# Kernel optimization log

Hardware: AMD Instinct MI355X
Metric: run time of the kernel (lower is better)

Reference implementation:

```python
import jax, jax.numpy as jnp
import numpy as np

N = 100000      # nodes == in_ch (transductive: x = arange(N))
E = 3200000     # nonzeros of sparse hypergraph adjacency G (COO)
D = 128         # i_emb
DROPOUT = 0.1


def setup_inputs() -> dict:
    key = jax.random.key(0)
    k1, k2, k3, k4, k5 = jax.random.split(key, 5)
    x = jnp.arange(N, dtype=jnp.int64) if jax.config.jax_enable_x64 else jnp.arange(N, dtype=jnp.int32)
    row = jax.random.randint(k1, (E,), 0, N, dtype=jnp.int32)
    col = jax.random.randint(k2, (E,), 0, N, dtype=jnp.int32)
    vals = jax.random.uniform(k3, (E,), dtype=jnp.float32)
    # xavier-uniform embedding: bound = sqrt(6/(N+D))
    eb = float(np.sqrt(6.0 / (N + D)))
    embed_w = jax.random.uniform(k4, (N, D), jnp.float32, -eb, eb)
    fb = float(np.sqrt(6.0 / (D + D)))
    fc_w = jax.random.uniform(k5, (D, D), jnp.float32, -fb, fb)
    fc_b = jnp.zeros((D,), jnp.float32)
    return {"x": x, "row": row, "col": col, "vals": vals,
            "embed_w": embed_w, "fc_w": fc_w, "fc_b": fc_b}


def reference(x, row, col, vals, embed_w, fc_w, fc_b):
    e = embed_w[x]                                   # [N, D] embedding lookup
    # SpMM: out[i] = sum_{nz} vals * e[col]  scattered to row
    agg = jax.ops.segment_sum(vals[:, None] * e[col], row, num_segments=e.shape[0])
    m1 = agg + e                                     # residual
    keep = 1.0 - DROPOUT                             # F.dropout (training=True default)
    mask = jax.random.bernoulli(jax.random.key(42), keep, m1.shape)
    m1 = jnp.where(mask, m1 / keep, 0.0)
    x1 = jax.nn.leaky_relu(m1 @ fc_w.T + fc_b, negative_slope=0.2)
    return jnp.concatenate((e, x1), axis=1)          # [N, 2D]
```

## Files before the change

kernel.cpp:

```cpp
#include <hip/hip_runtime.h>


#define NN 100000
#define DD 128
#define EE 3200000
#define NSUB (NN * 8)
#define S1B 1024
#define NBLK1 ((NSUB + S1B - 1) / S1B)

__device__ __forceinline__ unsigned rotl32(unsigned v, int s) {
    return (v << s) | (v >> (32 - s));
}

__device__ __forceinline__ bool keep_elem(unsigned idx) {
    unsigned x0 = 0u, x1 = idx;
    const unsigned k0 = 0u, k1 = 42u;
    const unsigned k2 = 0x1BD11BDAu ^ k0 ^ k1;
    x0 += k0; x1 += k1;
#define TFROUND(s) x0 += x1; x1 = rotl32(x1, s); x1 ^= x0;
    TFROUND(13) TFROUND(15) TFROUND(26) TFROUND(6)
    x0 += k1; x1 += k2 + 1u;
    TFROUND(17) TFROUND(29) TFROUND(16) TFROUND(24)
    x0 += k2; x1 += k0 + 2u;
    TFROUND(13) TFROUND(15) TFROUND(26) TFROUND(6)
    x0 += k0; x1 += k1 + 3u;
    TFROUND(17) TFROUND(29) TFROUND(16) TFROUND(24)
    x0 += k1; x1 += k2 + 4u;
    TFROUND(13) TFROUND(15) TFROUND(26) TFROUND(6)
    x0 += k2; x1 += k0 + 5u;
#undef TFROUND
    unsigned bits = x0 ^ x1;
    float u = __uint_as_float((bits >> 9) | 0x3f800000u) - 1.0f;
    return u < 0.9f;
}

__global__ __launch_bounds__(256) void setup_kernel(const float4* __restrict__ emb4,
                                                    uint2* __restrict__ ebf2,
                                                    int4* __restrict__ counts4) {
    int i = blockIdx.x * 256 + threadIdx.x;
    float4 v = emb4[i];
    unsigned a = __float_as_uint(v.x), b = __float_as_uint(v.y);
    unsigned c = __float_as_uint(v.z), d = __float_as_uint(v.w);
    a = (a + 0x7fffu + ((a >> 16) & 1u)) >> 16;
    b = (b + 0x7fffu + ((b >> 16) & 1u)) >> 16;
    c = (c + 0x7fffu + ((c >> 16) & 1u)) >> 16;
    d = (d + 0x7fffu + ((d >> 16) & 1u)) >> 16;
    uint2 o;
    o.x = a | (b << 16);
    o.y = c | (d << 16);
    ebf2[i] = o;
    if (i < NSUB / 4) counts4[i] = make_int4(0, 0, 0, 0);
}

__global__ __launch_bounds__(256) void hist_kernel(const int4* __restrict__ row4,
                                                   int* __restrict__ counts,
                                                   unsigned* __restrict__ rank4) {
    int i = blockIdx.x * 256 + threadIdx.x;
    int4 r = row4[i];
    int sb = (i & 1) << 2;
    unsigned k0 = (unsigned)atomicAdd(&counts[r.x * 8 + sb + 0], 1);
    unsigned k1 = (unsigned)atomicAdd(&counts[r.y * 8 + sb + 1], 1);
    unsigned k2 = (unsigned)atomicAdd(&counts[r.z * 8 + sb + 2], 1);
    unsigned k3 = (unsigned)atomicAdd(&counts[r.w * 8 + sb + 3], 1);
    rank4[i] = k0 | (k1 << 8) | (k2 << 16) | (k3 << 24);
}

__global__ __launch_bounds__(S1B) void scan1_kernel(const int* __restrict__ counts,
                                                    int* __restrict__ subptr,
                                                    int* __restrict__ bsums) {
    __shared__ int s[S1B];
    int t = threadIdx.x;
    int i = blockIdx.x * S1B + t;
    int v = (i < NSUB) ? counts[i] : 0;
    s[t] = v;
    __syncthreads();
    for (int d = 1; d < S1B; d <<= 1) {
        int a = (t >= d) ? s[t - d] : 0;
        __syncthreads();
        s[t] += a;
        __syncthreads();
    }
    if (i < NSUB) subptr[i + 1] = s[t];
    if (t == S1B - 1) bsums[blockIdx.x] = s[t];
}

__global__ __launch_bounds__(S1B) void scan2_kernel(int* __restrict__ bsums) {
    __shared__ int s[S1B];
    int t = threadIdx.x;
    int v = (t < NBLK1) ? bsums[t] : 0;
    s[t] = v;
    __syncthreads();
    for (int d = 1; d < S1B; d <<= 1) {
        int a = (t >= d) ? s[t - d] : 0;
        __syncthreads();
        s[t] += a;
        __syncthreads();
    }
    if (t < NBLK1) bsums[t] = s[t] - v;
}

__global__ __launch_bounds__(S1B) void scan3_kernel(int* __restrict__ subptr,
                                                    const int* __restrict__ bsums) {
    int i = blockIdx.x * S1B + threadIdx.x;
    if (i < NSUB) subptr[i + 1] += bsums[i >> 10];
    if (i == 0) subptr[0] = 0;
}

__device__ __forceinline__ unsigned pack_entry(int xc, float v) {
    unsigned pb = __float_as_uint(v) + 0x10000u;
    return (pb & 0xFFFE0000u) | (unsigned)xc;
}

__global__ __launch_bounds__(256) void fill_kernel(const int* __restrict__ x,
                                                   const int4* __restrict__ row4,
                                                   const int4* __restrict__ col4,
                                                   const float4* __restrict__ vals4,
                                                   const unsigned* __restrict__ rank4,
                                                   const int* __restrict__ subptr,
                                                   unsigned* __restrict__ csr) {
    int i = blockIdx.x * 256 + threadIdx.x;
    int4 r = row4[i];
    int4 c = col4[i];
    float4 v = vals4[i];
    unsigned kk = rank4[i];
    int sb = (i & 1) << 2;
    csr[subptr[r.x * 8 + sb + 0] + (kk & 0xffu)]         = pack_entry(x[c.x], v.x);
    csr[subptr[r.y * 8 + sb + 1] + ((kk >> 8) & 0xffu)]  = pack_entry(x[c.y], v.y);
    csr[subptr[r.z * 8 + sb + 2] + ((kk >> 16) & 0xffu)] = pack_entry(x[c.z], v.z);
    csr[subptr[r.w * 8 + sb + 3] + (kk >> 24)]           = pack_entry(x[c.w], v.w);
}

__global__ __launch_bounds__(256) void gather_kernel(const int* __restrict__ x,
                                                     const int* __restrict__ subptr,
                                                     const unsigned* __restrict__ csr,
                                                     const unsigned* __restrict__ ebf,
                                                     const float2* __restrict__ emb2,
                                                     float2* __restrict__ out2) {
    int wave = threadIdx.x >> 6;
    int lane = threadIdx.x & 63;
    int n = blockIdx.x * 4 + wave;
    int s = subptr[n * 8], e = subptr[n * 8 + 8];
    float ax = 0.f, ay = 0.f;
    int j = s;
    for (; j + 4 <= e; j += 4) {
        unsigned p0 = csr[j], p1 = csr[j + 1], p2 = csr[j + 2], p3 = csr[j + 3];
        unsigned b0 = ebf[(long)(p0 & 0x1FFFFu) * 64 + lane];
        unsigned b1 = ebf[(long)(p1 & 0x1FFFFu) * 64 + lane];
        unsigned b2 = ebf[(long)(p2 & 0x1FFFFu) * 64 + lane];
        unsigned b3 = ebf[(long)(p3 & 0x1FFFFu) * 64 + lane];
        float v0 = __uint_as_float(p0 & 0xFFFE0000u);
        float v1 = __uint_as_float(p1 & 0xFFFE0000u);
        float v2 = __uint_as_float(p2 & 0xFFFE0000u);
        float v3 = __uint_as_float(p3 & 0xFFFE0000u);
        ax += v0 * __uint_as_float(b0 << 16) + v1 * __uint_as_float(b1 << 16)
            + v2 * __uint_as_float(b2 << 16) + v3 * __uint_as_float(b3 << 16);
        ay += v0 * __uint_as_float(b0 & 0xffff0000u) + v1 * __uint_as_float(b1 & 0xffff0000u)
            + v2 * __uint_as_float(b2 & 0xffff0000u) + v3 * __uint_as_float(b3 & 0xffff0000u);
    }
    for (; j < e; ++j) {
        unsigned p = csr[j];
        unsigned b = ebf[(long)(p & 0x1FFFFu) * 64 + lane];
        float v = __uint_as_float(p & 0xFFFE0000u);
        ax += v * __uint_as_float(b << 16);
        ay += v * __uint_as_float(b & 0xffff0000u);
    }
    float2 es = emb2[(long)x[n] * 64 + lane];
    out2[(long)n * 128 + lane] = es;
    float2 m1;
    m1.x = ax + es.x;
    m1.y = ay + es.y;
    unsigned base = (unsigned)n * 128u + 2u * (unsigned)lane;
    m1.x = keep_elem(base) ? m1.x * (1.0f / 0.9f) : 0.0f;
    m1.y = keep_elem(base + 1u) ? m1.y * (1.0f / 0.9f) : 0.0f;
    out2[(long)n * 128 + 64 + lane] = m1;
}

__global__ __launch_bounds__(256, 3) void fc3_kernel(float* __restrict__ out,
                                                     const float* __restrict__ fc_w,
                                                     const float* __restrict__ fc_b) {
    __shared__ float ms_t[128][66];
    __shared__ float wc[32][132];
    int tid = threadIdx.x;
    int row0 = blockIdx.x * 64;
    const float4* fcw4 = (const float4*)fc_w;
    const float4* out4c = (const float4*)out;

    for (int chunk = tid; chunk < 64 * 32; chunk += 256) {
        int nl = chunk >> 5;
        int q = chunk & 31;
        int n = row0 + nl;
        float4 v = (n < NN) ? out4c[(long)n * 64 + 32 + q]
                            : make_float4(0.f, 0.f, 0.f, 0.f);
        ms_t[q * 4 + 0][nl] = v.x;
        ms_t[q * 4 + 1][nl] = v.y;
        ms_t[q * 4 + 2][nl] = v.z;
        ms_t[q * 4 + 3][nl] = v.w;
    }

    int cg = tid & 31;
    int rg = tid >> 5;
    float acc[8][4];
#pragma unroll
    for (int r = 0; r < 8; ++r)
#pragma unroll
        for (int c = 0; c < 4; ++c) acc[r][c] = 0.f;

    for (int ch = 0; ch < 4; ++ch) {
        __syncthreads();
        for (int chunk = tid; chunk < 128 * 8; chunk += 256) {
            int jj = chunk >> 3;
            int kq = chunk & 7;
            float4 v = fcw4[jj * 32 + ch * 8 + kq];
            wc[kq * 4 + 0][jj] = v.x;
            wc[kq * 4 + 1][jj] = v.y;
            wc[kq * 4 + 2][jj] = v.z;
            wc[kq * 4 + 3][jj] = v.w;
        }
        __syncthreads();
        int kbase = ch * 32;
#pragma unroll
        for (int kk = 0; kk < 32; ++kk) {
            float4 w4 = *(const float4*)(&wc[kk][cg * 4]);
            int k = kbase + kk;
            float2 m01 = *(const float2*)(&ms_t[k][rg * 8 + 0]);
            float2 m23 = *(const float2*)(&ms_t[k][rg * 8 + 2]);
            float2 m45 = *(const float2*)(&ms_t[k][rg * 8 + 4]);
            float2 m67 = *(const float2*)(&ms_t[k][rg * 8 + 6]);
            float m[8] = {m01.x, m01.y, m23.x, m23.y, m45.x, m45.y, m67.x, m67.y};
#pragma unroll
            for (int r = 0; r < 8; ++r) {
                acc[r][0] += m[r] * w4.x;
                acc[r][1] += m[r] * w4.y;
                acc[r][2] += m[r] * w4.z;
                acc[r][3] += m[r] * w4.w;
            }
        }
    }

    float4 b4 = *(const float4*)(fc_b + cg * 4);
#pragma unroll
    for (int r = 0; r < 8; ++r) {
        int n = row0 + rg * 8 + r;
        if (n >= NN) break;
        float4 o;
        o.x = acc[r][0] + b4.x;
        o.y = acc[r][1] + b4.y;
        o.z = acc[r][2] + b4.z;
        o.w = acc[r][3] + b4.w;
        o.x = o.x >= 0.f ? o.x : 0.2f * o.x;
        o.y = o.y >= 0.f ? o.y : 0.2f * o.y;
        o.z = o.z >= 0.f ? o.z : 0.2f * o.z;
        o.w = o.w >= 0.f ? o.w : 0.2f * o.w;
        *(float4*)(out + (long)n * 256 + 128 + cg * 4) = o;
    }
}

__global__ __launch_bounds__(256) void init_kernel(const int* __restrict__ x,
                                                   const float4* __restrict__ emb4,
                                                   float4* __restrict__ out4) {
    int i = blockIdx.x * 256 + threadIdx.x;
    int n = i >> 5;
    int q = i & 31;
    if (n >= NN) return;
    float4 v = emb4[(long)x[n] * 32 + q];
    out4[(long)n * 64 + q] = v;
    out4[(long)n * 64 + 32 + q] = v;
}

#define EDGES_PER_GROUP 8
__global__ __launch_bounds__(256) void scatter_kernel(const int* __restrict__ x,
                                                      const int* __restrict__ row,
                                                      const int* __restrict__ col,
                                                      const float* __restrict__ vals,
                                                      const float4* __restrict__ emb4,
                                                      float* __restrict__ out) {
    long gid = (long)blockIdx.x * 256 + threadIdx.x;
    long group = gid >> 5;
    int lane = (int)(gid & 31);
    long e0 = group * EDGES_PER_GROUP;
#pragma unroll
    for (int k = 0; k < EDGES_PER_GROUP; ++k) {
        long e = e0 + k;
        if (e >= EE) break;
        int r = row[e];
        int c = col[e];
        float v = vals[e];
        float4 ev = emb4[(long)x[c] * 32 + lane];
        float* dst = out + (long)r * 256 + 128 + lane * 4;
        atomicAdd(dst + 0, v * ev.x);
        atomicAdd(dst + 1, v * ev.y);
        atomicAdd(dst + 2, v * ev.z);
        atomicAdd(dst + 3, v * ev.w);
    }
}

__global__ __launch_bounds__(256) void fc_kernel(float* __restrict__ out,
                                                 const float* __restrict__ fc_w,
                                                 const float* __restrict__ fc_b) {
    __shared__ float wt[128][132];
    __shared__ float ms[32][128];
    int tid = threadIdx.x;
    int row0 = blockIdx.x * 32;

    for (int i = tid; i < 128 * 128; i += 256) {
        int j = i >> 7, k = i & 127;
        wt[k][j] = fc_w[i];
    }
    for (int i = tid; i < 32 * 32; i += 256) {
        int r = i >> 5, q = i & 31;
        long n = row0 + r;
        float4 v = *(const float4*)(out + n * 256 + 128 + q * 4);
        unsigned base = (unsigned)n * 128u + (unsigned)(q * 4);
        float* vp = reinterpret_cast<float*>(&v);
#pragma unroll
        for (int c = 0; c < 4; ++c)
            vp[c] = keep_elem(base + c) ? vp[c] * (1.0f / 0.9f) : 0.0f;
        *(float4*)(&ms[r][q * 4]) = v;
    }
    __syncthreads();

    int rg = tid >> 5;
    int cg = tid & 31;
    float acc[4][4] = {{0.f}};
    for (int k = 0; k < 128; ++k) {
        float4 w4 = *(const float4*)(&wt[k][cg * 4]);
#pragma unroll
        for (int r = 0; r < 4; ++r) {
            float m = ms[rg * 4 + r][k];
            acc[r][0] += m * w4.x;
            acc[r][1] += m * w4.y;
            acc[r][2] += m * w4.z;
            acc[r][3] += m * w4.w;
        }
    }

    float4 b4 = *(const float4*)(fc_b + cg * 4);
#pragma unroll
    for (int r = 0; r < 4; ++r) {
        long n = row0 + rg * 4 + r;
        float4 o;
        o.x = acc[r][0] + b4.x;
        o.y = acc[r][1] + b4.y;
        o.z = acc[r][2] + b4.z;
        o.w = acc[r][3] + b4.w;
        o.x = o.x >= 0.f ? o.x : 0.2f * o.x;
        o.y = o.y >= 0.f ? o.y : 0.2f * o.y;
        o.z = o.z >= 0.f ? o.z : 0.2f * o.z;
        o.w = o.w >= 0.f ? o.w : 0.2f * o.w;
        *(float4*)(out + n * 256 + 128 + cg * 4) = o;
    }
}

extern "C" void kernel_launch(void* const* d_in, const int* in_sizes, int n_in,
                              void* d_out, int out_size, void* d_ws, size_t ws_size,
                              hipStream_t stream) {
    const int*   x    = (const int*)d_in[0];
    const int*   row  = (const int*)d_in[1];
    const int*   col  = (const int*)d_in[2];
    const float* vals = (const float*)d_in[3];
    const float* emb  = (const float*)d_in[4];
    const float* fc_w = (const float*)d_in[5];
    const float* fc_b = (const float*)d_in[6];
    float* out = (float*)d_out;

    size_t off = 0;
    char* ws = (char*)d_ws;
    int* counts = (int*)(ws + off); off += (size_t)NSUB * 4;
    int* subptr = (int*)(ws + off); off += (((size_t)(NSUB + 1) * 4) + 255) & ~(size_t)255;
    int* bsums  = (int*)(ws + off); off += 4096;
    unsigned* csr = (unsigned*)(ws + off); off += (size_t)EE * 4;
    unsigned* rank = (unsigned*)(ws + off); off += (size_t)EE;
    unsigned* ebf = (unsigned*)(ws + off); off += (size_t)NN * DD * 2;
    size_t need = off;

    if (ws_size >= need) {
        setup_kernel<<<(int)(((long)NN * DD / 4 + 255) / 256), 256, 0, stream>>>(
            (const float4*)emb, (uint2*)ebf, (int4*)counts);
        hist_kernel<<<EE / 4 / 256, 256, 0, stream>>>((const int4*)row, counts, rank);
        scan1_kernel<<<NBLK1, S1B, 0, stream>>>(counts, subptr, bsums);
        scan2_kernel<<<1, S1B, 0, stream>>>(bsums);
        scan3_kernel<<<NBLK1, S1B, 0, stream>>>(subptr, bsums);
        fill_kernel<<<EE / 4 / 256, 256, 0, stream>>>(x, (const int4*)row, (const int4*)col,
                                                      (const float4*)vals, rank, subptr, csr);
        gather_kernel<<<NN / 4, 256, 0, stream>>>(x, subptr, csr, ebf,
                                                  (const float2*)emb, (float2*)out);
        fc3_kernel<<<(NN + 63) / 64, 256, 0, stream>>>(out, fc_w, fc_b);
    } else {
        init_kernel<<<(NN * 32 + 255) / 256, 256, 0, stream>>>(x, (const float4*)emb, (float4*)out);
        int scatter_blocks = (int)(((long)EE / EDGES_PER_GROUP) * 32 / 256);
        scatter_kernel<<<scatter_blocks, 256, 0, stream>>>(x, row, col, vals,
                                                           (const float4*)emb, out);
        fc_kernel<<<NN / 32, 256, 0, stream>>>(out, fc_w, fc_b);
    }
}
```

Measured before the change: 599.9 us.

## Replace global-atomic CSR build with two-pass bucketed radix partition

The COO-to-CSR conversion no longer uses per-edge global atomics into 800K sub-row counters. It now does a two-level partition: per-chunk shared-memory histograms over 391 row buckets, a scan, a scatter into buckets, and a per-bucket local sort in LDS that writes exact row pointers. This cuts global atomic contention and the separate rank array, at the cost of an extra pass over the edges and a fixed LDS capacity (CAP) per bucket that could overflow on skewed row distributions.

Result: faster. 531.3 us (-11.4%).

```diff
diff --git a/kernel.cpp b/kernel.cpp
--- a/kernel.cpp
+++ b/kernel.cpp
@@ -4,9 +4,13 @@
 #define NN 100000
 #define DD 128
 #define EE 3200000
-#define NSUB (NN * 8)
+#define NBKT 391
+#define NCHUNK 256
+#define CHUNK_E (EE / NCHUNK)
+#define NSUB2 (NBKT * NCHUNK)
 #define S1B 1024
-#define NBLK1 ((NSUB + S1B - 1) / S1B)
+#define NBLK2 ((NSUB2 + S1B - 1) / S1B)
+#define CAP 11264
 
 __device__ __forceinline__ unsigned rotl32(unsigned v, int s) {
     return (v << s) | (v >> (32 - s));
@@ -35,8 +39,7 @@
 }
 
 __global__ __launch_bounds__(256) void setup_kernel(const float4* __restrict__ emb4,
-                                                    uint2* __restrict__ ebf2,
-                                                    int4* __restrict__ counts4) {
+                                                    uint2* __restrict__ ebf2) {
     int i = blockIdx.x * 256 + threadIdx.x;
     float4 v = emb4[i];
     unsigned a = __float_as_uint(v.x), b = __float_as_uint(v.y);
@@ -49,29 +52,28 @@
     o.x = a | (b << 16);
     o.y = c | (d << 16);
     ebf2[i] = o;
-    if (i < NSUB / 4) counts4[i] = make_int4(0, 0, 0, 0);
-}
-
-__global__ __launch_bounds__(256) void hist_kernel(const int4* __restrict__ row4,
-                                                   int* __restrict__ counts,
-                                                   unsigned* __restrict__ rank4) {
-    int i = blockIdx.x * 256 + threadIdx.x;
-    int4 r = row4[i];
-    int sb = (i & 1) << 2;
-    unsigned k0 = (unsigned)atomicAdd(&counts[r.x * 8 + sb + 0], 1);
-    unsigned k1 = (unsigned)atomicAdd(&counts[r.y * 8 + sb + 1], 1);
-    unsigned k2 = (unsigned)atomicAdd(&counts[r.z * 8 + sb + 2], 1);
-    unsigned k3 = (unsigned)atomicAdd(&counts[r.w * 8 + sb + 3], 1);
-    rank4[i] = k0 | (k1 << 8) | (k2 << 16) | (k3 << 24);
-}
-
-__global__ __launch_bounds__(S1B) void scan1_kernel(const int* __restrict__ counts,
-                                                    int* __restrict__ subptr,
+}
+
+__global__ __launch_bounds__(256) void part1_kernel(const int* __restrict__ row,
+                                                    int* __restrict__ cnt) {
+    __shared__ int h[NBKT];
+    int t = threadIdx.x, c = blockIdx.x;
+    for (int b = t; b < NBKT; b += 256) h[b] = 0;
+    __syncthreads();
+    int e0 = c * CHUNK_E;
+    for (int e = e0 + t; e < e0 + CHUNK_E; e += 256)
+        atomicAdd(&h[row[e] >> 8], 1);
+    __syncthreads();
+    for (int b = t; b < NBKT; b += 256) cnt[b * NCHUNK + c] = h[b];
+}
+
+__global__ __launch_bounds__(S1B) void scan1_kernel(const int* __restrict__ cnt,
+                                                    int* __restrict__ ofsX,
                                                     int* __restrict__ bsums) {
     __shared__ int s[S1B];
     int t = threadIdx.x;
     int i = blockIdx.x * S1B + t;
-    int v = (i < NSUB) ? counts[i] : 0;
+    int v = (i < NSUB2) ? cnt[i] : 0;
     s[t] = v;
     __syncthreads();
     for (int d = 1; d < S1B; d <<= 1) {
@@ -80,14 +82,14 @@
         s[t] += a;
         __syncthreads();
     }
-    if (i < NSUB) subptr[i + 1] = s[t];
+    if (i < NSUB2) ofsX[i + 1] = s[t];
     if (t == S1B - 1) bsums[blockIdx.x] = s[t];
 }
 
 __global__ __launch_bounds__(S1B) void scan2_kernel(int* __restrict__ bsums) {
     __shared__ int s[S1B];
     int t = threadIdx.x;
-    int v = (t < NBLK1) ? bsums[t] : 0;
+    int v = (t < NBLK2) ? bsums[t] : 0;
     s[t] = v;
     __syncthreads();
     for (int d = 1; d < S1B; d <<= 1) {
@@ -96,14 +98,14 @@
         s[t] += a;
         __syncthreads();
     }
-    if (t < NBLK1) bsums[t] = s[t] - v;
-}
-
-__global__ __launch_bounds__(S1B) void scan3_kernel(int* __restrict__ subptr,
+    if (t < NBLK2) bsums[t] = s[t] - v;
+}
+
+__global__ __launch_bounds__(S1B) void scan3_kernel(int* __restrict__ ofsX,
                                                     const int* __restrict__ bsums) {
     int i = blockIdx.x * S1B + threadIdx.x;
-    if (i < NSUB) subptr[i + 1] += bsums[i >> 10];
-    if (i == 0) subptr[0] = 0;
+    if (i < NSUB2) ofsX[i + 1] += bsums[i >> 10];
+    if (i == 0) ofsX[0] = 0;
 }
 
 __device__ __forceinline__ unsigned pack_entry(int xc, float v) {
@@ -111,27 +113,69 @@
     return (pb & 0xFFFE0000u) | (unsigned)xc;
 }
 
-__global__ __launch_bounds__(256) void fill_kernel(const int* __restrict__ x,
-                                                   const int4* __restrict__ row4,
-                                                   const int4* __restrict__ col4,
-                                                   const float4* __restrict__ vals4,
-                                                   const unsigned* __restrict__ rank4,
-                                                   const int* __restrict__ subptr,
-                                                   unsigned* __restrict__ csr) {
-    int i = blockIdx.x * 256 + threadIdx.x;
-    int4 r = row4[i];
-    int4 c = col4[i];
-    float4 v = vals4[i];
-    unsigned kk = rank4[i];
-    int sb = (i & 1) << 2;
-    csr[subptr[r.x * 8 + sb + 0] + (kk & 0xffu)]         = pack_entry(x[c.x], v.x);
-    csr[subptr[r.y * 8 + sb + 1] + ((kk >> 8) & 0xffu)]  = pack_entry(x[c.y], v.y);
-    csr[subptr[r.z * 8 + sb + 2] + ((kk >> 16) & 0xffu)] = pack_entry(x[c.z], v.z);
-    csr[subptr[r.w * 8 + sb + 3] + (kk >> 24)]           = pack_entry(x[c.w], v.w);
+__global__ __launch_bounds__(256) void part2_kernel(const int* __restrict__ x,
+                                                    const int* __restrict__ row,
+                                                    const int* __restrict__ col,
+                                                    const float* __restrict__ vals,
+                                                    const int* __restrict__ ofsX,
+                                                    unsigned* __restrict__ ebkt,
+                                                    unsigned char* __restrict__ rbkt) {
+    __shared__ int offs[NBKT];
+    int t = threadIdx.x, c = blockIdx.x;
+    for (int b = t; b < NBKT; b += 256) offs[b] = ofsX[b * NCHUNK + c];
+    __syncthreads();
+    int e0 = c * CHUNK_E;
+    for (int e = e0 + t; e < e0 + CHUNK_E; e += 256) {
+        int r = row[e];
+        int pos = atomicAdd(&offs[r >> 8], 1);
+        ebkt[pos] = pack_entry(x[col[e]], vals[e]);
+        rbkt[pos] = (unsigned char)(r & 255);
+    }
+}
+
+__global__ __launch_bounds__(256) void part3_kernel(const int* __restrict__ ofsX,
+                                                    unsigned* __restrict__ ebkt,
+                                                    const unsigned char* __restrict__ rbkt,
+                                                    int* __restrict__ rowptr) {
+    __shared__ unsigned esh[CAP];
+    __shared__ unsigned char rsh[CAP];
+    __shared__ int h[256];
+    __shared__ int s[256];
+    int t = threadIdx.x, b = blockIdx.x;
+    int base = ofsX[b * NCHUNK];
+    int end  = ofsX[(b + 1) * NCHUNK];
+    int cnt_b = end - base;
+    h[t] = 0;
+    __syncthreads();
+    for (int k = t; k < cnt_b; k += 256) {
+        esh[k] = ebkt[base + k];
+        unsigned char r = rbkt[base + k];
+        rsh[k] = r;
+        atomicAdd(&h[r], 1);
+    }
+    __syncthreads();
+    int v = h[t];
+    s[t] = v;
+    __syncthreads();
+    for (int d = 1; d < 256; d <<= 1) {
+        int a = (t >= d) ? s[t - d] : 0;
+        __syncthreads();
+        s[t] += a;
+        __syncthreads();
+    }
+    int excl = s[t] - v;
+    int n = b * 256 + t;
+    if (n <= NN) rowptr[n] = base + excl;
+    h[t] = base + excl;
+    __syncthreads();
+    for (int k = t; k < cnt_b; k += 256) {
+        int pos = atomicAdd(&h[rsh[k]], 1);
+        ebkt[pos] = esh[k];
+    }
 }
 
 __global__ __launch_bounds__(256) void gather_kernel(const int* __restrict__ x,
-                                                     const int* __restrict__ subptr,
+                                                     const int* __restrict__ rowptr,
                                                      const unsigned* __restrict__ csr,
                                                      const unsigned* __restrict__ ebf,
                                                      const float2* __restrict__ emb2,
@@ -139,7 +183,7 @@
     int wave = threadIdx.x >> 6;
     int lane = threadIdx.x & 63;
     int n = blockIdx.x * 4 + wave;
-    int s = subptr[n * 8], e = subptr[n * 8 + 8];
+    int s = rowptr[n], e = rowptr[n + 1];
     float ax = 0.f, ay = 0.f;
     int j = s;
     for (; j + 4 <= e; j += 4) {
@@ -365,24 +409,25 @@
 
     size_t off = 0;
     char* ws = (char*)d_ws;
-    int* counts = (int*)(ws + off); off += (size_t)NSUB * 4;
-    int* subptr = (int*)(ws + off); off += (((size_t)(NSUB + 1) * 4) + 255) & ~(size_t)255;
+    int* cnt    = (int*)(ws + off); off += 400640;
+    int* ofsX   = (int*)(ws + off); off += 400640;
     int* bsums  = (int*)(ws + off); off += 4096;
-    unsigned* csr = (unsigned*)(ws + off); off += (size_t)EE * 4;
-    unsigned* rank = (unsigned*)(ws + off); off += (size_t)EE;
+    int* rowptr = (int*)(ws + off); off += 400128;
+    unsigned* ebkt = (unsigned*)(ws + off); off += (size_t)EE * 4;
+    unsigned char* rbkt = (unsigned char*)(ws + off); off += (size_t)EE;
     unsigned* ebf = (unsigned*)(ws + off); off += (size_t)NN * DD * 2;
     size_t need = off;
 
     if (ws_size >= need) {
-        setup_kernel<<<(int)(((long)NN * DD / 4 + 255) / 256), 256, 0, stream>>>(
-            (const float4*)emb, (uint2*)ebf, (int4*)counts);
-        hist_kernel<<<EE / 4 / 256, 256, 0, stream>>>((const int4*)row, counts, rank);
-        scan1_kernel<<<NBLK1, S1B, 0, stream>>>(counts, subptr, bsums);
+        setup_kernel<<<(int)((long)NN * DD / 4 / 256), 256, 0, stream>>>(
+            (const float4*)emb, (uint2*)ebf);
+        part1_kernel<<<NCHUNK, 256, 0, stream>>>(row, cnt);
+        scan1_kernel<<<NBLK2, S1B, 0, stream>>>(cnt, ofsX, bsums);
         scan2_kernel<<<1, S1B, 0, stream>>>(bsums);
-        scan3_kernel<<<NBLK1, S1B, 0, stream>>>(subptr, bsums);
-        fill_kernel<<<EE / 4 / 256, 256, 0, stream>>>(x, (const int4*)row, (const int4*)col,
-                                                      (const float4*)vals, rank, subptr, csr);
-        gather_kernel<<<NN / 4, 256, 0, stream>>>(x, subptr, csr, ebf,
+        scan3_kernel<<<NBLK2, S1B, 0, stream>>>(ofsX, bsums);
+        part2_kernel<<<NCHUNK, 256, 0, stream>>>(x, row, col, vals, ofsX, ebkt, rbkt);
+        part3_kernel<<<NBKT, 256, 0, stream>>>(ofsX, ebkt, rbkt, rowptr);
+        gather_kernel<<<NN / 4, 256, 0, stream>>>(x, rowptr, ebkt, ebf,
                                                   (const float2*)emb, (float2*)out);
         fc3_kernel<<<(NN + 63) / 64, 256, 0, stream>>>(out, fc_w, fc_b);
     } else {
```
